# Kernel optimization log

Hardware: AMD Instinct MI355X
Metric: run time of the kernel (lower is better)

The kernel has to match this reference:

```python
import jax, jax.numpy as jnp
import numpy as np

B_, T_, IDIM, D, H, FF, L, MAXLEN = 8, 512, 1799, 256, 4, 2048, 16, 1000
DK = D // H


def _ln(x, g, b, eps=1e-12):
    m = jnp.mean(x, axis=-1, keepdims=True)
    v = jnp.mean((x - m) ** 2, axis=-1, keepdims=True)
    return (x - m) * jax.lax.rsqrt(v + eps) * g + b


def setup_inputs() -> dict:
    key = jax.random.key(0)
    ks = jax.random.split(key, 16)
    s = 0.02
    n = lambda k, shape: jax.random.normal(k, shape, jnp.float32) * s
    return {
        'xs': jax.random.normal(ks[0], (B_, T_, IDIM), jnp.float32),
        'masks': jnp.ones((B_, 1, T_), jnp.int32),
        'emb_w': n(ks[1], (D, IDIM)), 'emb_b': jnp.zeros((D,), jnp.float32),
        'emb_g': jnp.ones((D,), jnp.float32), 'emb_beta': jnp.zeros((D,), jnp.float32),
        'pe_k': n(ks[2], (2 * MAXLEN, DK)),
        'Wq': n(ks[3], (L, D, D)), 'bq': jnp.zeros((L, D), jnp.float32),
        'Wk': n(ks[4], (L, D, D)), 'bk': jnp.zeros((L, D), jnp.float32),
        'Wv': n(ks[5], (L, D, D)), 'bv': jnp.zeros((L, D), jnp.float32),
        'Wo': n(ks[6], (L, D, D)), 'bo': jnp.zeros((L, D), jnp.float32),
        'ln1_g': jnp.ones((L, D), jnp.float32), 'ln1_b': jnp.zeros((L, D), jnp.float32),
        'ln2_g': jnp.ones((L, D), jnp.float32), 'ln2_b': jnp.zeros((L, D), jnp.float32),
        'lnk_g': jnp.ones((L, DK), jnp.float32), 'lnk_b': jnp.zeros((L, DK), jnp.float32),
        'W1': n(ks[7], (L, FF, D)), 'b1': jnp.zeros((L, FF), jnp.float32),
        'W2': n(ks[8], (L, D, FF)), 'b2': jnp.zeros((L, D), jnp.float32),
        'after_g': jnp.ones((D,), jnp.float32), 'after_b': jnp.zeros((D,), jnp.float32),
    }


def reference(xs, masks, emb_w, emb_b, emb_g, emb_beta, pe_k, Wq, bq, Wk, bk, Wv, bv, Wo, bo,
              ln1_g, ln1_b, ln2_g, ln2_b, lnk_g, lnk_b, W1, b1, W2, b2, after_g, after_b):
    # embed: Linear -> LayerNorm -> (Dropout=id) -> ReLU
    x = jax.nn.relu(_ln(xs @ emb_w.T + emb_b, emb_g, emb_beta))  # [B,T,D]
    # relative position table gather: pos_k [T,T,DK]
    pos = jnp.arange(T_)
    rel = jnp.clip(pos[:, None] - pos[None, :], -MAXLEN, MAXLEN - 1) + MAXLEN
    pos_k = pe_k[rel]
    neg = (masks == 0)[:, None, :, :]  # [B,1,1,T]
    minval = jnp.finfo(x.dtype).min
    scale = 1.0 / np.sqrt(DK).astype(np.float32)

    def block(x, p):
        y = _ln(x, p['ln1_g'], p['ln1_b'])
        pk = _ln(pos_k, p['lnk_g'], p['lnk_b'])  # norm_k applied per layer
        proj = lambda W, b: (y @ W.T + b).reshape(B_, T_, H, DK).transpose(0, 2, 1, 3)
        q = proj(p['Wq'], p['bq'])  # [B,H,T,DK]
        k = proj(p['Wk'], p['bk'])
        v = proj(p['Wv'], p['bv'])
        A = jnp.einsum('bhtd,bhsd->bhts', q, k)
        Bt = jnp.einsum('bhtd,tsd->bhts', q, pk)  # rel-pos bias term
        scores = jnp.where(neg, minval, (A + Bt) * scale)
        attn = jnp.where(neg, 0.0, jax.nn.softmax(scores, axis=-1))
        o = jnp.einsum('bhts,bhsd->bhtd', attn, v)
        o = o.transpose(0, 2, 1, 3).reshape(B_, T_, D)
        x = x + o @ p['Wo'].T + p['bo']
        y2 = _ln(x, p['ln2_g'], p['ln2_b'])
        ff = jax.nn.relu(y2 @ p['W1'].T + p['b1']) @ p['W2'].T + p['b2']
        return x + ff, None

    params = {'Wq': Wq, 'bq': bq, 'Wk': Wk, 'bk': bk, 'Wv': Wv, 'bv': bv, 'Wo': Wo, 'bo': bo,
              'ln1_g': ln1_g, 'ln1_b': ln1_b, 'ln2_g': ln2_g, 'ln2_b': ln2_b,
              'lnk_g': lnk_g, 'lnk_b': lnk_b, 'W1': W1, 'b1': b1, 'W2': W2, 'b2': b2}
    x, _ = jax.lax.scan(block, x, params)
    return _ln(x, after_g, after_b)
```

## Files before the change

### kernel.cpp

```cpp
#include <hip/hip_runtime.h>
#include <cstdint>


typedef __bf16 bf16_t;
typedef bf16_t bf16x4 __attribute__((ext_vector_type(4)));
typedef bf16_t bf16x8 __attribute__((ext_vector_type(8)));
typedef float  f32x4  __attribute__((ext_vector_type(4)));

#define B_    8
#define T_    512
#define IDIM  1799
#define KPAD  1856
#define D_    256
#define H_    4
#define DK    64
#define FF_   2048
#define L_    16
#define NROW  4096
#define PKROWS 2000
#define NBH   32
#define NSA   4

__device__ __forceinline__ f32x4 mfma16(bf16x8 a, bf16x8 b, f32x4 c) {
  return __builtin_amdgcn_mfma_f32_16x16x32_bf16(a, b, c, 0, 0, 0);
}

__device__ __forceinline__ void async_cp16(const void* g, void* l) {
  __builtin_amdgcn_global_load_lds(
      (__attribute__((address_space(1))) void*)(g),
      (__attribute__((address_space(3))) void*)(l), 16, 0, 0);
}

__global__ __launch_bounds__(256) void cvt_f32_bf16(const float* __restrict__ s,
                                                    bf16_t* __restrict__ d, int n) {
  int i = blockIdx.x * 256 + threadIdx.x;
  int stride = gridDim.x * 256;
  for (; i < n; i += stride) d[i] = (bf16_t)s[i];
}

__global__ __launch_bounds__(256) void cvt_pad_row(const float* __restrict__ s,
                                                   bf16_t* __restrict__ d,
                                                   int ksrc, int kdst) {
  const int r = blockIdx.x;
  const float* sr = s + (size_t)r * ksrc;
  bf16_t* dr = d + (size_t)r * kdst;
  for (int k = threadIdx.x; k < kdst; k += 256)
    dr[k] = (k < ksrc) ? (bf16_t)sr[k] : (bf16_t)0.f;
}

__global__ __launch_bounds__(256) void pack_qkvw(const float* __restrict__ wq,
                                                 const float* __restrict__ wk,
                                                 const float* __restrict__ wv,
                                                 bf16_t* __restrict__ dst) {
  const int per_l = 768 * 256;
  int i = blockIdx.x * 256 + threadIdx.x;
  int stride = gridDim.x * 256;
  for (; i < L_ * per_l; i += stride) {
    int l = i / per_l, r = i - l * per_l;
    int n = r >> 8, c = r & 255;
    int sel = n >> 8, nn = n & 255;
    const float* w = (sel == 0) ? wq : (sel == 1) ? wk : wv;
    dst[i] = (bf16_t)w[((size_t)l * 256 + nn) * 256 + c];
  }
}

__global__ __launch_bounds__(256) void pack_qkvb(const float* __restrict__ bq,
                                                 const float* __restrict__ bk,
                                                 const float* __restrict__ bv,
                                                 float* __restrict__ dst) {
  int i = blockIdx.x * 256 + threadIdx.x;
  if (i >= L_ * 768) return;
  int l = i / 768, n = i - l * 768;
  int sel = n >> 8, nn = n & 255;
  const float* b = (sel == 0) ? bq : (sel == 1) ? bk : bv;
  dst[i] = b[l * 256 + nn];
}

__global__ __launch_bounds__(256) void pkn_ln(const float* __restrict__ pe_k,
                                              const float* __restrict__ lnk_g,
                                              const float* __restrict__ lnk_b,
                                              bf16_t* __restrict__ out) {
  const int idx = blockIdx.x * 4 + (threadIdx.x >> 6);
  if (idx >= L_ * PKROWS) return;
  const int lane = threadIdx.x & 63;
  const int l = idx / PKROWS, r = idx - l * PKROWS;
  float v = pe_k[(size_t)r * DK + lane];
  float s = v;
#pragma unroll
  for (int o = 32; o; o >>= 1) s += __shfl_xor(s, o);
  const float mean = s * (1.f / DK);
  const float dx = v - mean;
  float q = dx * dx;
#pragma unroll
  for (int o = 32; o; o >>= 1) q += __shfl_xor(q, o);
  const float rs = rsqrtf(q * (1.f / DK) + 1e-12f);
  out[((size_t)l * PKROWS + r) * DK + lane] =
      (bf16_t)(dx * rs * lnk_g[l * DK + lane] + lnk_b[l * DK + lane]);
}

__global__ __launch_bounds__(256) void ln_rows_f32(const float* __restrict__ src,
                                                   const float* __restrict__ g,
                                                   const float* __restrict__ b,
                                                   float* __restrict__ dst) {
  const int row = blockIdx.x * 4 + (threadIdx.x >> 6);
  const int lane = threadIdx.x & 63;
  const float4 v = ((const float4*)(src + (size_t)row * D_))[lane];
  float s = v.x + v.y + v.z + v.w;
#pragma unroll
  for (int o = 32; o; o >>= 1) s += __shfl_xor(s, o);
  const float mean = s * (1.f / D_);
  const float d0 = v.x - mean, d1 = v.y - mean, d2 = v.z - mean, d3 = v.w - mean;
  float q = d0 * d0 + d1 * d1 + d2 * d2 + d3 * d3;
#pragma unroll
  for (int o = 32; o; o >>= 1) q += __shfl_xor(q, o);
  const float rs = rsqrtf(q * (1.f / D_) + 1e-12f);
  const float4 gg = ((const float4*)g)[lane];
  const float4 bb = ((const float4*)b)[lane];
  ((float4*)(dst + (size_t)row * D_))[lane] =
      make_float4(d0 * rs * gg.x + bb.x, d1 * rs * gg.y + bb.y,
                  d2 * rs * gg.z + bb.z, d3 * rs * gg.w + bb.w);
}

template <int NS, bool WRITE_Y>
__global__ __launch_bounds__(256) void add_combine_ln(
    const float* __restrict__ parts, const float* __restrict__ bias,
    float* __restrict__ x, const float* __restrict__ g,
    const float* __restrict__ b, bf16_t* __restrict__ y) {
  const int row = blockIdx.x * 4 + (threadIdx.x >> 6);
  const int lane = threadIdx.x & 63;
  const size_t idx = (size_t)row * 64 + lane;
  float4 v = ((const float4*)x)[idx];
#pragma unroll
  for (int p = 0; p < NS; ++p) {
    float4 pv = ((const float4*)parts)[(size_t)p * NROW * 64 + idx];
    v.x += pv.x; v.y += pv.y; v.z += pv.z; v.w += pv.w;
  }
  const float4 bi = ((const float4*)bias)[lane];
  v.x += bi.x; v.y += bi.y; v.z += bi.z; v.w += bi.w;
  ((float4*)x)[idx] = v;
  if (WRITE_Y) {
    float s = v.x + v.y + v.z + v.w;
#pragma unroll
    for (int o = 32; o; o >>= 1) s += __shfl_xor(s, o);
    const float mean = s * (1.f / D_);
    const float d0 = v.x - mean, d1 = v.y - mean, d2 = v.z - mean, d3 = v.w - mean;
    float q = d0 * d0 + d1 * d1 + d2 * d2 + d3 * d3;
#pragma unroll
    for (int o = 32; o; o >>= 1) q += __shfl_xor(q, o);
    const float rs = rsqrtf(q * (1.f / D_) + 1e-12f);
    const float4 gg = ((const float4*)g)[lane];
    const float4 bb = ((const float4*)b)[lane];
    bf16x4 o4 = {(bf16_t)(d0 * rs * gg.x + bb.x), (bf16_t)(d1 * rs * gg.y + bb.y),
                 (bf16_t)(d2 * rs * gg.z + bb.z), (bf16_t)(d3 * rs * gg.w + bb.w)};
    ((bf16x4*)y)[idx] = o4;
  }
}

__global__ __launch_bounds__(256) void embed_combine(
    const float* __restrict__ parts, const float* __restrict__ bias,
    const float* __restrict__ g0, const float* __restrict__ b0,
    const float* __restrict__ g1, const float* __restrict__ b1,
    float* __restrict__ x, bf16_t* __restrict__ y) {
  const int row = blockIdx.x * 4 + (threadIdx.x >> 6);
  const int lane = threadIdx.x & 63;
  const size_t idx = (size_t)row * 64 + lane;
  float4 v = ((const float4*)parts)[idx];
#pragma unroll
  for (int p = 1; p < 4; ++p) {
    float4 pv = ((const float4*)parts)[(size_t)p * NROW * 64 + idx];
    v.x += pv.x; v.y += pv.y; v.z += pv.z; v.w += pv.w;
  }
  const float4 bi = ((const float4*)bias)[lane];
  v.x += bi.x; v.y += bi.y; v.z += bi.z; v.w += bi.w;
  float s = v.x + v.y + v.z + v.w;
#pragma unroll
  for (int o = 32; o; o >>= 1) s += __shfl_xor(s, o);
  float mean = s * (1.f / D_);
  float d0 = v.x - mean, d1 = v.y - mean, d2 = v.z - mean, d3 = v.w - mean;
  float q = d0 * d0 + d1 * d1 + d2 * d2 + d3 * d3;
#pragma unroll
  for (int o = 32; o; o >>= 1) q += __shfl_xor(q, o);
  float rs = rsqrtf(q * (1.f / D_) + 1e-12f);
  const float4 gg = ((const float4*)g0)[lane];
  const float4 bb = ((const float4*)b0)[lane];
  float x0 = fmaxf(d0 * rs * gg.x + bb.x, 0.f);
  float x1 = fmaxf(d1 * rs * gg.y + bb.y, 0.f);
  float x2 = fmaxf(d2 * rs * gg.z + bb.z, 0.f);
  float x3 = fmaxf(d3 * rs * gg.w + bb.w, 0.f);
  ((float4*)x)[idx] = make_float4(x0, x1, x2, x3);
  s = x0 + x1 + x2 + x3;
#pragma unroll
  for (int o = 32; o; o >>= 1) s += __shfl_xor(s, o);
  mean = s * (1.f / D_);
  d0 = x0 - mean; d1 = x1 - mean; d2 = x2 - mean; d3 = x3 - mean;
  q = d0 * d0 + d1 * d1 + d2 * d2 + d3 * d3;
#pragma unroll
  for (int o = 32; o; o >>= 1) q += __shfl_xor(q, o);
  rs = rsqrtf(q * (1.f / D_) + 1e-12f);
  const float4 g1v = ((const float4*)g1)[lane];
  const float4 b1v = ((const float4*)b1)[lane];
  bf16x4 o4 = {(bf16_t)(d0 * rs * g1v.x + b1v.x), (bf16_t)(d1 * rs * g1v.y + b1v.y),
               (bf16_t)(d2 * rs * g1v.z + b1v.z), (bf16_t)(d3 * rs * g1v.w + b1v.w)};
  ((bf16x4*)y)[idx] = o4;
}

template <int BM, int BN, int EP, int MINW>
__global__ __launch_bounds__(256, MINW) void gemm_bf16(
    const bf16_t* __restrict__ A, int lda, const bf16_t* __restrict__ B, int ldb,
    const float* __restrict__ bias, void* __restrict__ Cout, int ldc,
    int K, size_t zstride) {
  constexpr int HM = BM / 2, HN = BN / 2;
  constexpr int FM = HM / 16, FN = HN / 16;
  constexpr int CA = (BM * 8) / 256, CB = (BN * 8) / 256;
  __shared__ bf16_t lsA[BM * 64];
  __shared__ bf16_t lsB[BN * 64];
  const int tid = threadIdx.x;
  const int w = tid >> 6, lane = tid & 63;
  const int wm = w >> 1, wn = w & 1;
  const int lanelo = lane & 15, quad = lane >> 4;
  const int wbase = tid & ~63;
  const int m0 = blockIdx.x * BM, n0 = blockIdx.y * BN;
  const int ktiles = K >> 6;
  const int tpz = (ktiles + gridDim.z - 1) / gridDim.z;
  const int kb = blockIdx.z * tpz * 64;
  const int ke = min(K, kb + tpz * 64);
  f32x4 acc[FM][FN] = {};

  for (int kt = kb; kt < ke; kt += 64) {
    __syncthreads();
#pragma unroll
    for (int rr = 0; rr < CA; ++rr) {
      int chunk = rr * 256 + tid;
      int r = chunk >> 3, c8 = chunk & 7;
      int lg = c8 ^ (r & 7);
      async_cp16(A + (size_t)(m0 + r) * lda + kt + lg * 8,
                 lsA + (size_t)(rr * 256 + wbase) * 8);
    }
#pragma unroll
    for (int rr = 0; rr < CB; ++rr) {
      int chunk = rr * 256 + tid;
      int r = chunk >> 3, c8 = chunk & 7;
      int lg = c8 ^ (r & 7);
      async_cp16(B + (size_t)(n0 + r) * ldb + kt + lg * 8,
                 lsB + (size_t)(rr * 256 + wbase) * 8);
    }
    __syncthreads();
    bf16x8 af[FM][2], bfv[FN][2];
#pragma unroll
    for (int i = 0; i < FM; ++i) {
      int r = wm * HM + i * 16 + lanelo;
#pragma unroll
      for (int kk = 0; kk < 2; ++kk)
        af[i][kk] = *(const bf16x8*)(lsA + (size_t)(r * 8 + ((kk * 4 + quad) ^ (r & 7))) * 8);
    }
#pragma unroll
    for (int j = 0; j < FN; ++j) {
      int r = wn * HN + j * 16 + lanelo;
#pragma unroll
      for (int kk = 0; kk < 2; ++kk)
        bfv[j][kk] = *(const bf16x8*)(lsB + (size_t)(r * 8 + ((kk * 4 + quad) ^ (r & 7))) * 8);
    }
#pragma unroll
    for (int kk = 0; kk < 2; ++kk)
#pragma unroll
      for (int i = 0; i < FM; ++i)
#pragma unroll
        for (int j = 0; j < FN; ++j)
          acc[i][j] = mfma16(af[i][kk], bfv[j][kk], acc[i][j]);
  }

#pragma unroll
  for (int i = 0; i < FM; ++i) {
#pragma unroll
    for (int j = 0; j < FN; ++j) {
#pragma unroll
      for (int reg = 0; reg < 4; ++reg) {
        const int m = m0 + wm * HM + i * 16 + quad * 4 + reg;
        const int n = n0 + wn * HN + j * 16 + lanelo;
        const size_t idx = (size_t)m * ldc + n;
        if constexpr (EP == 4) {
          ((float*)Cout + (size_t)blockIdx.z * zstride)[idx] = acc[i][j][reg];
        } else {
          float v = acc[i][j][reg] + bias[n];
          if constexpr (EP == 1) {
            ((bf16_t*)Cout)[idx] = (bf16_t)v;
          } else {
            ((bf16_t*)Cout)[idx] = (bf16_t)fmaxf(v, 0.f);
          }
        }
      }
    }
  }
}

__global__ __launch_bounds__(256, 2) void wo_gemm(
    const bf16_t* __restrict__ Opart, const float* __restrict__ mpart,
    const float* __restrict__ lpart, const bf16_t* __restrict__ B,
    float* __restrict__ Cout, size_t zstride) {
  __shared__ bf16_t lsA[64 * 64];
  __shared__ bf16_t lsB[128 * 64];
  const int tid = threadIdx.x;
  const int w = tid >> 6, lane = tid & 63;
  const int wm = w >> 1, wn = w & 1;
  const int lanelo = lane & 15, quad = lane >> 4;
  const int wbase = tid & ~63;
  const int m0 = blockIdx.x * 64, n0 = blockIdx.y * 128;
  const int z = blockIdx.z;
  const int bb = m0 >> 9, t0 = m0 & 511;
  f32x4 acc[2][4] = {};

  for (int kt = z * 128; kt < z * 128 + 128; kt += 64) {
    __syncthreads();
    const int hh = kt >> 6;
    const int bh = bb * 4 + hh;
#pragma unroll
    for (int rr = 0; rr < 2; ++rr) {
      int chunk = rr * 256 + tid;
      int r = chunk >> 3, c8 = chunk & 7;
      int dk0 = (c8 ^ (r & 7)) * 8;
      int t = t0 + r;
      float mp[NSA], lp[NSA];
      float mmax = -__builtin_inff();
#pragma unroll
      for (int p = 0; p < NSA; ++p) {
        const size_t prow = ((size_t)p * NBH + bh) * T_ + t;
        mp[p] = mpart[prow]; lp[p] = lpart[prow];
        mmax = fmaxf(mmax, mp[p]);
      }
      float e[NSA], denom = 0.f;
#pragma unroll
      for (int p = 0; p < NSA; ++p) {
        e[p] = __expf(mp[p] - mmax);
        denom += lp[p] * e[p];
      }
      const float inv = (denom > 0.f) ? 1.f / denom : 0.f;
      float cv[8] = {};
#pragma unroll
      for (int p = 0; p < NSA; ++p) {
        const float wgt = e[p] * inv;
        bf16x8 op = *(const bf16x8*)(Opart +
            (((size_t)p * NBH + bh) * T_ + t) * 64 + dk0);
#pragma unroll
        for (int i = 0; i < 8; ++i) cv[i] += wgt * (float)op[i];
      }
      bf16x8 rv;
#pragma unroll
      for (int i = 0; i < 8; ++i) rv[i] = (bf16_t)cv[i];
      *(bf16x8*)(lsA + (size_t)chunk * 8) = rv;
    }
#pragma unroll
    for (int rr = 0; rr < 4; ++rr) {
      int chunk = rr * 256 + tid;
      int r = chunk >> 3, c8 = chunk & 7;
      int lg = c8 ^ (r & 7);
      async_cp16(B + (size_t)(n0 + r) * 256 + kt + lg * 8,
                 lsB + (size_t)(rr * 256 + wbase) * 8);
    }
    __syncthreads();
    bf16x8 af[2][2], bfv[4][2];
#pragma unroll
    for (int i = 0; i < 2; ++i) {
      int r = wm * 32 + i * 16 + lanelo;
#pragma unroll
      for (int kk = 0; kk < 2; ++kk)
        af[i][kk] = *(const bf16x8*)(lsA + (size_t)(r * 8 + ((kk * 4 + quad) ^ (r & 7))) * 8);
    }
#pragma unroll
    for (int j = 0; j < 4; ++j) {
      int r = wn * 64 + j * 16 + lanelo;
#pragma unroll
      for (int kk = 0; kk < 2; ++kk)
        bfv[j][kk] = *(const bf16x8*)(lsB + (size_t)(r * 8 + ((kk * 4 + quad) ^ (r & 7))) * 8);
    }
#pragma unroll
    for (int kk = 0; kk < 2; ++kk)
#pragma unroll
      for (int i = 0; i < 2; ++i)
#pragma unroll
        for (int j = 0; j < 4; ++j)
          acc[i][j] = mfma16(af[i][kk], bfv[j][kk], acc[i][j]);
  }

#pragma unroll
  for (int i = 0; i < 2; ++i)
#pragma unroll
    for (int j = 0; j < 4; ++j)
#pragma unroll
      for (int reg = 0; reg < 4; ++reg) {
        const int m = m0 + wm * 32 + i * 16 + quad * 4 + reg;
        const int n = n0 + wn * 64 + j * 16 + lanelo;
        (Cout + (size_t)z * zstride)[(size_t)m * D_ + n] = acc[i][j][reg];
      }
}

__global__ __launch_bounds__(256, 3) void attn_fused(
    const bf16_t* __restrict__ qkv, const bf16_t* __restrict__ pkn,
    const int* __restrict__ masks, bf16_t* __restrict__ Opart,
    float* __restrict__ mpart, float* __restrict__ lpart) {
  __shared__ bf16_t ls_qp[64 * 72];
  __shared__ bf16_t ls_pkr[64 * 196];
  __shared__ bf16_t ls_k[64 * 64];
  __shared__ bf16_t ls_vt[64 * 72];

  const int tid = threadIdx.x, w = tid >> 6, lane = tid & 63;
  const int lanelo = lane & 15, quad = lane >> 4;
  const int wbase = tid & ~63;
  const int t0 = blockIdx.x * 64;
  const int bh = blockIdx.y, bb = bh >> 2, h = bh & 3;
  const int z = blockIdx.z;
  const size_t rowbase = (size_t)bb * T_;
  const int jb = t0 - 128 * z + 873;

#pragma unroll
  for (int rr = 0; rr < 2; ++rr) {
    int chunk = rr * 256 + tid;
    int r = chunk >> 3, c8 = chunk & 7;
    int lg = c8 ^ (r & 7);
    async_cp16(qkv + (rowbase + t0 + r) * 768 + h * 64 + lg * 8,
               ls_qp + (size_t)(rr * 256 + wbase) * 8);
  }
#pragma unroll
  for (int rr = 0; rr < 6; ++rr) {
    int chunk = rr * 256 + tid;
    int r = chunk >> 3, c8 = chunk & 7;
    int lg = c8 ^ (r & 7);
    async_cp16(pkn + (size_t)(jb + r) * DK + lg * 8,
               ls_pkr + (size_t)(rr * 256 + wbase) * 8);
  }
  __syncthreads();
  bf16x8 qf[2];
#pragma unroll
  for (int kk = 0; kk < 2; ++kk) {
    int r = w * 16 + lanelo;
    qf[kk] = *(const bf16x8*)(ls_qp + (size_t)(r * 8 + ((kk * 4 + quad) ^ (r & 7))) * 8);
  }
  f32x4 racc[12] = {};
#pragma unroll
  for (int kk = 0; kk < 2; ++kk)
#pragma unroll
    for (int nf = 0; nf < 12; ++nf) {
      int r = nf * 16 + lanelo;
      bf16x8 bj = *(const bf16x8*)(ls_pkr + (size_t)(r * 8 + ((kk * 4 + quad) ^ (r & 7))) * 8);
      racc[nf] = mfma16(qf[kk], bj, racc[nf]);
    }
  __syncthreads();
#pragma unroll
  for (int nf = 0; nf < 12; ++nf)
#pragma unroll
    for (int reg = 0; reg < 4; ++reg)
      ls_pkr[(w * 16 + quad * 4 + reg) * 196 + nf * 16 + lanelo] =
          (bf16_t)racc[nf][reg];

  f32x4 o_acc[4] = {};
  float m_run[4], l_run[4];
#pragma unroll
  for (int i = 0; i < 4; ++i) { m_run[i] = -__builtin_inff(); l_run[i] = 0.f; }

  for (int stl = 0; stl < 2; ++stl) {
    const int s0 = 128 * z + 64 * stl;
    __syncthreads();
#pragma unroll
    for (int rr = 0; rr < 2; ++rr) {
      int chunk = rr * 256 + tid;
      int r = chunk >> 3, c8 = chunk & 7;
      int lg = c8 ^ (r & 7);
      async_cp16(qkv + (rowbase + s0 + r) * 768 + 256 + h * 64 + lg * 8,
                 ls_k + (size_t)(rr * 256 + wbase) * 8);
    }
#pragma unroll
    for (int c = tid; c < 64 * 8; c += 256) {
      int r = c & 63, d0 = (c >> 6) * 8;
      bf16x8 vv = *(const bf16x8*)(qkv + (rowbase + s0 + r) * 768 + 512 + h * 64 + d0);
#pragma unroll
      for (int i = 0; i < 8; ++i) ls_vt[(d0 + i) * 72 + r] = vv[i];
    }
    int mk[4];
#pragma unroll
    for (int nf = 0; nf < 4; ++nf)
      mk[nf] = masks[bb * T_ + s0 + nf * 16 + lanelo];
    __syncthreads();

    f32x4 sacc[4] = {};
#pragma unroll
// ... 60 lines not shown
#pragma unroll
    for (int nf = 0; nf < 4; ++nf)
      Opart[prow * 64 + nf * 16 + lanelo] = (bf16_t)o_acc[nf][reg];
    if (lanelo == 0) { mpart[prow] = m_run[reg]; lpart[prow] = l_run[reg]; }
  }
}

extern "C" void kernel_launch(void* const* d_in, const int* in_sizes, int n_in,
                              void* d_out, int out_size, void* d_ws, size_t ws_size,
                              hipStream_t stream) {
  const float* xs       = (const float*)d_in[0];
  const int*   masks    = (const int*)d_in[1];
  const float* emb_w    = (const float*)d_in[2];
  const float* emb_b    = (const float*)d_in[3];
  const float* emb_g    = (const float*)d_in[4];
  const float* emb_beta = (const float*)d_in[5];
  const float* pe_k     = (const float*)d_in[6];
  const float* Wq       = (const float*)d_in[7];
  const float* bq       = (const float*)d_in[8];
  const float* Wk       = (const float*)d_in[9];
  const float* bk       = (const float*)d_in[10];
  const float* Wv       = (const float*)d_in[11];
  const float* bv       = (const float*)d_in[12];
  const float* Wo       = (const float*)d_in[13];
  const float* bo       = (const float*)d_in[14];
  const float* ln1_g    = (const float*)d_in[15];
  const float* ln1_b    = (const float*)d_in[16];
  const float* ln2_g    = (const float*)d_in[17];
  const float* ln2_b    = (const float*)d_in[18];
  const float* lnk_g    = (const float*)d_in[19];
  const float* lnk_b    = (const float*)d_in[20];
  const float* W1       = (const float*)d_in[21];
  const float* b1       = (const float*)d_in[22];
  const float* W2       = (const float*)d_in[23];
  const float* b2       = (const float*)d_in[24];
  const float* after_g  = (const float*)d_in[25];
  const float* after_b  = (const float*)d_in[26];

  char* ws = (char*)d_ws;
  size_t off = 0;
  auto take = [&](size_t bytes) -> void* {
    void* p = ws + off;
    off += (bytes + 255) & ~(size_t)255;
    return p;
  };
  bf16_t* ewb  = (bf16_t*)take((size_t)D_ * KPAD * 2);
  bf16_t* wcat = (bf16_t*)take((size_t)L_ * 768 * D_ * 2);
  float*  bcat = (float*) take((size_t)L_ * 768 * 4);
  bf16_t* wob  = (bf16_t*)take((size_t)L_ * D_ * D_ * 2);
  bf16_t* w1b  = (bf16_t*)take((size_t)L_ * FF_ * D_ * 2);
  bf16_t* w2b  = (bf16_t*)take((size_t)L_ * D_ * FF_ * 2);
  bf16_t* pknb = (bf16_t*)take((size_t)L_ * PKROWS * DK * 2);
  float*  x    = (float*) take((size_t)NROW * D_ * 4);
  bf16_t* y    = (bf16_t*)take((size_t)NROW * D_ * 2);
  bf16_t* qkv  = (bf16_t*)take((size_t)NROW * 768 * 2);
  bf16_t* hbuf = (bf16_t*)take((size_t)NROW * FF_ * 2);
  bf16_t* Opart = (bf16_t*)take((size_t)NSA * NBH * T_ * 64 * 2);
  float*  mpart = (float*)take((size_t)NSA * NBH * T_ * 4);
  float*  lpart = (float*)take((size_t)NSA * NBH * T_ * 4);
  float*  gpart = (float*)take((size_t)4 * NROW * D_ * 4);
  bf16_t* xsb  = hbuf;
  const size_t ZS = (size_t)NROW * D_;

  cvt_pad_row<<<NROW, 256, 0, stream>>>(xs, xsb, IDIM, KPAD);
  cvt_pad_row<<<D_, 256, 0, stream>>>(emb_w, ewb, IDIM, KPAD);
  pack_qkvw<<<2048, 256, 0, stream>>>(Wq, Wk, Wv, wcat);
  pack_qkvb<<<48, 256, 0, stream>>>(bq, bk, bv, bcat);
  cvt_f32_bf16<<<1024, 256, 0, stream>>>(Wo, wob, L_ * D_ * D_);
  cvt_f32_bf16<<<2048, 256, 0, stream>>>(W1, w1b, L_ * FF_ * D_);
  cvt_f32_bf16<<<2048, 256, 0, stream>>>(W2, w2b, L_ * D_ * FF_);
  pkn_ln<<<(L_ * PKROWS) / 4, 256, 0, stream>>>(pe_k, lnk_g, lnk_b, pknb);

  gemm_bf16<128, 128, 4, 2><<<dim3(NROW / 128, D_ / 128, 4), 256, 0, stream>>>(
      xsb, KPAD, ewb, KPAD, nullptr, gpart, D_, KPAD, ZS);
  embed_combine<<<NROW / 4, 256, 0, stream>>>(gpart, emb_b, emb_g, emb_beta,
                                              ln1_g, ln1_b, x, y);

  for (int l = 0; l < L_; ++l) {
    gemm_bf16<64, 128, 1, 3><<<dim3(NROW / 64, 768 / 128), 256, 0, stream>>>(
        y, D_, wcat + (size_t)l * 768 * D_, D_, bcat + l * 768, qkv, 768, D_, 0);
    attn_fused<<<dim3(T_ / 64, NBH, NSA), 256, 0, stream>>>(
        qkv, pknb + (size_t)l * PKROWS * DK, masks, Opart, mpart, lpart);
    wo_gemm<<<dim3(NROW / 64, D_ / 128, 2), 256, 0, stream>>>(
        Opart, mpart, lpart, wob + (size_t)l * D_ * D_, gpart, ZS);
    add_combine_ln<2, true><<<NROW / 4, 256, 0, stream>>>(
        gpart, bo + l * D_, x, ln2_g + l * D_, ln2_b + l * D_, y);
    gemm_bf16<128, 128, 2, 2><<<dim3(NROW / 128, FF_ / 128), 256, 0, stream>>>(
        y, D_, w1b + (size_t)l * FF_ * D_, D_, b1 + l * FF_, hbuf, FF_, D_, 0);
    gemm_bf16<128, 128, 4, 2><<<dim3(NROW / 128, D_ / 128, 4), 256, 0, stream>>>(
        hbuf, FF_, w2b + (size_t)l * D_ * FF_, FF_, nullptr, gpart, D_, FF_, ZS);
    if (l < L_ - 1) {
      add_combine_ln<4, true><<<NROW / 4, 256, 0, stream>>>(
          gpart, b2 + l * D_, x, ln1_g + (l + 1) * D_, ln1_b + (l + 1) * D_, y);
    } else {
      add_combine_ln<4, false><<<NROW / 4, 256, 0, stream>>>(
          gpart, b2 + l * D_, x, nullptr, nullptr, nullptr);
    }
  }
  ln_rows_f32<<<NROW / 4, 256, 0, stream>>>(x, after_g, after_b, (float*)d_out);
}
```

Baseline: 1.333 ms.

## Fuse LayerNorm into GEMM prologues and residual adds into GEMM epilogues

Removes the separate add/LayerNorm combine kernels. The QKV and FF1 GEMMs now normalise fp32 rows of x into LDS themselves. The Wo GEMM merges the attention split partials and adds bias and residual straight into x, and the FF2 GEMM uses split-K with atomicAdd into x. The weight conversion and packing kernels are merged into a single prep launch. The cost is that LayerNorm is recomputed for every N tile, tiles shrink to 64x64, and fp32 atomics make summation order non-deterministic.

```diff
diff --git a/kernel.cpp b/kernel.cpp
--- a/kernel.cpp
+++ b/kernel.cpp
@@ -31,11 +31,47 @@
       (__attribute__((address_space(3))) void*)(l), 16, 0, 0);
 }
 
-__global__ __launch_bounds__(256) void cvt_f32_bf16(const float* __restrict__ s,
-                                                    bf16_t* __restrict__ d, int n) {
-  int i = blockIdx.x * 256 + threadIdx.x;
-  int stride = gridDim.x * 256;
-  for (; i < n; i += stride) d[i] = (bf16_t)s[i];
+#define WCAT_N (L_ * 768 * 256)
+#define WOB_N  (L_ * 256 * 256)
+#define W1B_N  (L_ * 2048 * 256)
+#define W2B_N  (L_ * 256 * 2048)
+#define BCAT_N (L_ * 768)
+#define PREP_TOT (WCAT_N + WOB_N + W1B_N + W2B_N + BCAT_N)
+
+__global__ __launch_bounds__(256) void prep_all(
+    const float* __restrict__ wq, const float* __restrict__ wk,
+    const float* __restrict__ wv, const float* __restrict__ wo,
+    const float* __restrict__ w1, const float* __restrict__ w2,
+    const float* __restrict__ bq, const float* __restrict__ bk,
+    const float* __restrict__ bv, bf16_t* __restrict__ wcat,
+    bf16_t* __restrict__ wob, bf16_t* __restrict__ w1b,
+    bf16_t* __restrict__ w2b, float* __restrict__ bcat) {
+  const int stride = gridDim.x * 256;
+  for (int i = blockIdx.x * 256 + threadIdx.x; i < PREP_TOT; i += stride) {
+    int j = i;
+    if (j < WCAT_N) {
+      const int per_l = 768 * 256;
+      int l = j / per_l, r = j - l * per_l;
+      int n = r >> 8, c = r & 255;
+      int sel = n >> 8, nn = n & 255;
+      const float* wsrc = (sel == 0) ? wq : (sel == 1) ? wk : wv;
+      wcat[j] = (bf16_t)wsrc[((size_t)l * 256 + nn) * 256 + c];
+      continue;
+    }
+    j -= WCAT_N;
+    if (j < WOB_N) { wob[j] = (bf16_t)wo[j]; continue; }
+    j -= WOB_N;
+    if (j < W1B_N) { w1b[j] = (bf16_t)w1[j]; continue; }
+    j -= W1B_N;
+    if (j < W2B_N) { w2b[j] = (bf16_t)w2[j]; continue; }
+    j -= W2B_N;
+    {
+      int l = j / 768, n = j - l * 768;
+      int sel = n >> 8, nn = n & 255;
+      const float* bsrc = (sel == 0) ? bq : (sel == 1) ? bk : bv;
+      bcat[j] = bsrc[l * 256 + nn];
+    }
+  }
 }
 
 __global__ __launch_bounds__(256) void cvt_pad_row(const float* __restrict__ s,
@@ -46,34 +82,6 @@
   bf16_t* dr = d + (size_t)r * kdst;
   for (int k = threadIdx.x; k < kdst; k += 256)
     dr[k] = (k < ksrc) ? (bf16_t)sr[k] : (bf16_t)0.f;
-}
-
-__global__ __launch_bounds__(256) void pack_qkvw(const float* __restrict__ wq,
-                                                 const float* __restrict__ wk,
-                                                 const float* __restrict__ wv,
-                                                 bf16_t* __restrict__ dst) {
-  const int per_l = 768 * 256;
-  int i = blockIdx.x * 256 + threadIdx.x;
-  int stride = gridDim.x * 256;
-  for (; i < L_ * per_l; i += stride) {
-    int l = i / per_l, r = i - l * per_l;
-    int n = r >> 8, c = r & 255;
-    int sel = n >> 8, nn = n & 255;
-    const float* w = (sel == 0) ? wq : (sel == 1) ? wk : wv;
-    dst[i] = (bf16_t)w[((size_t)l * 256 + nn) * 256 + c];
-  }
-}
-
-__global__ __launch_bounds__(256) void pack_qkvb(const float* __restrict__ bq,
-                                                 const float* __restrict__ bk,
-                                                 const float* __restrict__ bv,
-                                                 float* __restrict__ dst) {
-  int i = blockIdx.x * 256 + threadIdx.x;
-  if (i >= L_ * 768) return;
-  int l = i / 768, n = i - l * 768;
-  int sel = n >> 8, nn = n & 255;
-  const float* b = (sel == 0) ? bq : (sel == 1) ? bk : bv;
-  dst[i] = b[l * 256 + nn];
 }
 
 __global__ __launch_bounds__(256) void pkn_ln(const float* __restrict__ pe_k,
@@ -121,46 +129,10 @@
                   d2 * rs * gg.z + bb.z, d3 * rs * gg.w + bb.w);
 }
 
-template <int NS, bool WRITE_Y>
-__global__ __launch_bounds__(256) void add_combine_ln(
-    const float* __restrict__ parts, const float* __restrict__ bias,
-    float* __restrict__ x, const float* __restrict__ g,
-    const float* __restrict__ b, bf16_t* __restrict__ y) {
-  const int row = blockIdx.x * 4 + (threadIdx.x >> 6);
-  const int lane = threadIdx.x & 63;
-  const size_t idx = (size_t)row * 64 + lane;
-  float4 v = ((const float4*)x)[idx];
-#pragma unroll
-  for (int p = 0; p < NS; ++p) {
-    float4 pv = ((const float4*)parts)[(size_t)p * NROW * 64 + idx];
-    v.x += pv.x; v.y += pv.y; v.z += pv.z; v.w += pv.w;
-  }
-  const float4 bi = ((const float4*)bias)[lane];
-  v.x += bi.x; v.y += bi.y; v.z += bi.z; v.w += bi.w;
-  ((float4*)x)[idx] = v;
-  if (WRITE_Y) {
-    float s = v.x + v.y + v.z + v.w;
-#pragma unroll
-    for (int o = 32; o; o >>= 1) s += __shfl_xor(s, o);
-    const float mean = s * (1.f / D_);
-    const float d0 = v.x - mean, d1 = v.y - mean, d2 = v.z - mean, d3 = v.w - mean;
-    float q = d0 * d0 + d1 * d1 + d2 * d2 + d3 * d3;
-#pragma unroll
-    for (int o = 32; o; o >>= 1) q += __shfl_xor(q, o);
-    const float rs = rsqrtf(q * (1.f / D_) + 1e-12f);
-    const float4 gg = ((const float4*)g)[lane];
-    const float4 bb = ((const float4*)b)[lane];
-    bf16x4 o4 = {(bf16_t)(d0 * rs * gg.x + bb.x), (bf16_t)(d1 * rs * gg.y + bb.y),
-                 (bf16_t)(d2 * rs * gg.z + bb.z), (bf16_t)(d3 * rs * gg.w + bb.w)};
-    ((bf16x4*)y)[idx] = o4;
-  }
-}
-
 __global__ __launch_bounds__(256) void embed_combine(
     const float* __restrict__ parts, const float* __restrict__ bias,
     const float* __restrict__ g0, const float* __restrict__ b0,
-    const float* __restrict__ g1, const float* __restrict__ b1,
-    float* __restrict__ x, bf16_t* __restrict__ y) {
+    float* __restrict__ x) {
   const int row = blockIdx.x * 4 + (threadIdx.x >> 6);
   const int lane = threadIdx.x & 63;
   const size_t idx = (size_t)row * 64 + lane;
@@ -175,43 +147,23 @@
   float s = v.x + v.y + v.z + v.w;
 #pragma unroll
   for (int o = 32; o; o >>= 1) s += __shfl_xor(s, o);
-  float mean = s * (1.f / D_);
-  float d0 = v.x - mean, d1 = v.y - mean, d2 = v.z - mean, d3 = v.w - mean;
+  const float mean = s * (1.f / D_);
+  const float d0 = v.x - mean, d1 = v.y - mean, d2 = v.z - mean, d3 = v.w - mean;
   float q = d0 * d0 + d1 * d1 + d2 * d2 + d3 * d3;
 #pragma unroll
   for (int o = 32; o; o >>= 1) q += __shfl_xor(q, o);
-  float rs = rsqrtf(q * (1.f / D_) + 1e-12f);
+  const float rs = rsqrtf(q * (1.f / D_) + 1e-12f);
   const float4 gg = ((const float4*)g0)[lane];
   const float4 bb = ((const float4*)b0)[lane];
-  float x0 = fmaxf(d0 * rs * gg.x + bb.x, 0.f);
-  float x1 = fmaxf(d1 * rs * gg.y + bb.y, 0.f);
-  float x2 = fmaxf(d2 * rs * gg.z + bb.z, 0.f);
-  float x3 = fmaxf(d3 * rs * gg.w + bb.w, 0.f);
-  ((float4*)x)[idx] = make_float4(x0, x1, x2, x3);
-  s = x0 + x1 + x2 + x3;
-#pragma unroll
-  for (int o = 32; o; o >>= 1) s += __shfl_xor(s, o);
-  mean = s * (1.f / D_);
-  d0 = x0 - mean; d1 = x1 - mean; d2 = x2 - mean; d3 = x3 - mean;
-  q = d0 * d0 + d1 * d1 + d2 * d2 + d3 * d3;
-#pragma unroll
-  for (int o = 32; o; o >>= 1) q += __shfl_xor(q, o);
-  rs = rsqrtf(q * (1.f / D_) + 1e-12f);
-  const float4 g1v = ((const float4*)g1)[lane];
-  const float4 b1v = ((const float4*)b1)[lane];
-  bf16x4 o4 = {(bf16_t)(d0 * rs * g1v.x + b1v.x), (bf16_t)(d1 * rs * g1v.y + b1v.y),
-               (bf16_t)(d2 * rs * g1v.z + b1v.z), (bf16_t)(d3 * rs * g1v.w + b1v.w)};
-  ((bf16x4*)y)[idx] = o4;
-}
-
-template <int BM, int BN, int EP, int MINW>
-__global__ __launch_bounds__(256, MINW) void gemm_bf16(
-    const bf16_t* __restrict__ A, int lda, const bf16_t* __restrict__ B, int ldb,
-    const float* __restrict__ bias, void* __restrict__ Cout, int ldc,
-    int K, size_t zstride) {
-  constexpr int HM = BM / 2, HN = BN / 2;
-  constexpr int FM = HM / 16, FN = HN / 16;
-  constexpr int CA = (BM * 8) / 256, CB = (BN * 8) / 256;
+  ((float4*)x)[idx] = make_float4(
+      fmaxf(d0 * rs * gg.x + bb.x, 0.f), fmaxf(d1 * rs * gg.y + bb.y, 0.f),
+      fmaxf(d2 * rs * gg.z + bb.z, 0.f), fmaxf(d3 * rs * gg.w + bb.w, 0.f));
+}
+
+__global__ __launch_bounds__(256, 2) void gemm_embed(
+    const bf16_t* __restrict__ A, const bf16_t* __restrict__ B,
+    float* __restrict__ Cout, size_t zstride) {
+  constexpr int BM = 128, BN = 128;
   __shared__ bf16_t lsA[BM * 64];
   __shared__ bf16_t lsB[BN * 64];
   const int tid = threadIdx.x;
@@ -220,42 +172,42 @@
   const int lanelo = lane & 15, quad = lane >> 4;
   const int wbase = tid & ~63;
   const int m0 = blockIdx.x * BM, n0 = blockIdx.y * BN;
-  const int ktiles = K >> 6;
-  const int tpz = (ktiles + gridDim.z - 1) / gridDim.z;
+  const int ktiles = KPAD >> 6;
+  const int tpz = (ktiles + 3) / 4;
   const int kb = blockIdx.z * tpz * 64;
-  const int ke = min(K, kb + tpz * 64);
-  f32x4 acc[FM][FN] = {};
+  const int ke = min(KPAD, kb + tpz * 64);
+  f32x4 acc[4][4] = {};
 
   for (int kt = kb; kt < ke; kt += 64) {
     __syncthreads();
 #pragma unroll
-    for (int rr = 0; rr < CA; ++rr) {
+    for (int rr = 0; rr < 4; ++rr) {
       int chunk = rr * 256 + tid;
       int r = chunk >> 3, c8 = chunk & 7;
       int lg = c8 ^ (r & 7);
-      async_cp16(A + (size_t)(m0 + r) * lda + kt + lg * 8,
+      async_cp16(A + (size_t)(m0 + r) * KPAD + kt + lg * 8,
                  lsA + (size_t)(rr * 256 + wbase) * 8);
     }
 #pragma unroll
-    for (int rr = 0; rr < CB; ++rr) {
+    for (int rr = 0; rr < 4; ++rr) {
       int chunk = rr * 256 + tid;
       int r = chunk >> 3, c8 = chunk & 7;
       int lg = c8 ^ (r & 7);
-      async_cp16(B + (size_t)(n0 + r) * ldb + kt + lg * 8,
+      async_cp16(B + (size_t)(n0 + r) * KPAD + kt + lg * 8,
                  lsB + (size_t)(rr * 256 + wbase) * 8);
     }
     __syncthreads();
-    bf16x8 af[FM][2], bfv[FN][2];
-#pragma unroll
-    for (int i = 0; i < FM; ++i) {
-      int r = wm * HM + i * 16 + lanelo;
+    bf16x8 af[4][2], bfv[4][2];
+#pragma unroll
+    for (int i = 0; i < 4; ++i) {
+      int r = wm * 64 + i * 16 + lanelo;
 #pragma unroll
       for (int kk = 0; kk < 2; ++kk)
         af[i][kk] = *(const bf16x8*)(lsA + (size_t)(r * 8 + ((kk * 4 + quad) ^ (r & 7))) * 8);
     }
 #pragma unroll
-    for (int j = 0; j < FN; ++j) {
-      int r = wn * HN + j * 16 + lanelo;
+    for (int j = 0; j < 4; ++j) {
+      int r = wn * 64 + j * 16 + lanelo;
 #pragma unroll
       for (int kk = 0; kk < 2; ++kk)
         bfv[j][kk] = *(const bf16x8*)(lsB + (size_t)(r * 8 + ((kk * 4 + quad) ^ (r & 7))) * 8);
@@ -263,101 +215,279 @@
 #pragma unroll
     for (int kk = 0; kk < 2; ++kk)
 #pragma unroll
-      for (int i = 0; i < FM; ++i)
-#pragma unroll
-        for (int j = 0; j < FN; ++j)
+      for (int i = 0; i < 4; ++i)
+#pragma unroll
+        for (int j = 0; j < 4; ++j)
           acc[i][j] = mfma16(af[i][kk], bfv[j][kk], acc[i][j]);
   }
-
-#pragma unroll
-  for (int i = 0; i < FM; ++i) {
-#pragma unroll
-    for (int j = 0; j < FN; ++j) {
+#pragma unroll
+  for (int i = 0; i < 4; ++i)
+#pragma unroll
+    for (int j = 0; j < 4; ++j)
 #pragma unroll
       for (int reg = 0; reg < 4; ++reg) {
-        const int m = m0 + wm * HM + i * 16 + quad * 4 + reg;
-        const int n = n0 + wn * HN + j * 16 + lanelo;
-        const size_t idx = (size_t)m * ldc + n;
-        if constexpr (EP == 4) {
-          ((float*)Cout + (size_t)blockIdx.z * zstride)[idx] = acc[i][j][reg];
-        } else {
-          float v = acc[i][j][reg] + bias[n];
-          if constexpr (EP == 1) {
-            ((bf16_t*)Cout)[idx] = (bf16_t)v;
-          } else {
-            ((bf16_t*)Cout)[idx] = (bf16_t)fmaxf(v, 0.f);
-          }
-        }
-      }
-    }
-  }
-}
-
-__global__ __launch_bounds__(256, 2) void wo_gemm(
-    const bf16_t* __restrict__ Opart, const float* __restrict__ mpart,
-    const float* __restrict__ lpart, const bf16_t* __restrict__ B,
-    float* __restrict__ Cout, size_t zstride) {
-  __shared__ bf16_t lsA[64 * 64];
-  __shared__ bf16_t lsB[128 * 64];
+        const int m = m0 + wm * 64 + i * 16 + quad * 4 + reg;
+        const int n = n0 + wn * 64 + j * 16 + lanelo;
+        (Cout + (size_t)blockIdx.z * zstride)[(size_t)m * D_ + n] =
+            acc[i][j][reg];
+      }
+}
+
+template <int EP>
+__global__ __launch_bounds__(256, 2) void gemm_ln(
+    const float* __restrict__ X, const float* __restrict__ g,
+    const float* __restrict__ b, const bf16_t* __restrict__ Bw,
+    const float* __restrict__ bias, bf16_t* __restrict__ Cout, int ldc) {
+  __shared__ bf16_t lsA[64 * 256];
+  __shared__ bf16_t lsB[64 * 256];
   const int tid = threadIdx.x;
   const int w = tid >> 6, lane = tid & 63;
   const int wm = w >> 1, wn = w & 1;
   const int lanelo = lane & 15, quad = lane >> 4;
   const int wbase = tid & ~63;
-  const int m0 = blockIdx.x * 64, n0 = blockIdx.y * 128;
+  const int m0 = blockIdx.x * 64, n0 = blockIdx.y * 64;
+
+#pragma unroll
+  for (int rr = 0; rr < 8; ++rr) {
+    int ch = rr * 256 + tid;
+    int r = ch >> 5, kb = (ch >> 3) & 3, c = ch & 7;
+    int lg = c ^ (r & 7);
+    async_cp16(Bw + (size_t)(n0 + r) * 256 + kb * 64 + lg * 8,
+               lsB + (size_t)(rr * 256 + wbase) * 8);
+  }
+  {
+    const int ar = tid >> 2, aq = tid & 3;
+    const float4* xrow = (const float4*)(X + (size_t)(m0 + ar) * 256) + aq * 16;
+    float4 xv[16];
+    float sum = 0.f;
+#pragma unroll
+    for (int i = 0; i < 16; ++i) {
+      xv[i] = xrow[i];
+      sum += xv[i].x + xv[i].y + xv[i].z + xv[i].w;
+    }
+    sum += __shfl_xor(sum, 1);
+    sum += __shfl_xor(sum, 2);
+    const float mean = sum * (1.f / 256.f);
+    float ss = 0.f;
+#pragma unroll
+    for (int i = 0; i < 16; ++i) {
+      float a0 = xv[i].x - mean, a1 = xv[i].y - mean;
+      float a2 = xv[i].z - mean, a3 = xv[i].w - mean;
+      ss += a0 * a0 + a1 * a1 + a2 * a2 + a3 * a3;
+    }
+    ss += __shfl_xor(ss, 1);
+    ss += __shfl_xor(ss, 2);
+    const float rs = rsqrtf(ss * (1.f / 256.f) + 1e-12f);
+    const float4* gg4 = (const float4*)g + aq * 16;
+    const float4* bb4 = (const float4*)b + aq * 16;
+#pragma unroll
+    for (int c = 0; c < 8; ++c) {
+      float4 v0 = xv[c * 2], v1 = xv[c * 2 + 1];
+      float4 g0 = gg4[c * 2], g1 = gg4[c * 2 + 1];
+      float4 b0 = bb4[c * 2], b1 = bb4[c * 2 + 1];
+      bf16x8 o;
+      o[0] = (bf16_t)((v0.x - mean) * rs * g0.x + b0.x);
+      o[1] = (bf16_t)((v0.y - mean) * rs * g0.y + b0.y);
+      o[2] = (bf16_t)((v0.z - mean) * rs * g0.z + b0.z);
+      o[3] = (bf16_t)((v0.w - mean) * rs * g0.w + b0.w);
+      o[4] = (bf16_t)((v1.x - mean) * rs * g1.x + b1.x);
+      o[5] = (bf16_t)((v1.y - mean) * rs * g1.y + b1.y);
+      o[6] = (bf16_t)((v1.z - mean) * rs * g1.z + b1.z);
+      o[7] = (bf16_t)((v1.w - mean) * rs * g1.w + b1.w);
+      *(bf16x8*)(lsA + (size_t)ar * 256 + (aq * 8 + ((c + ar) & 7)) * 8) = o;
+    }
+  }
+  __syncthreads();
+
+  f32x4 acc[2][2] = {};
+#pragma unroll
+  for (int kb = 0; kb < 4; ++kb) {
+    bf16x8 af[2][2], bfv[2][2];
+#pragma unroll
+    for (int i = 0; i < 2; ++i) {
+      int r = wm * 32 + i * 16 + lanelo;
+#pragma unroll
+      for (int kk = 0; kk < 2; ++kk)
+        af[i][kk] = *(const bf16x8*)(lsA + (size_t)r * 256 +
+                                     (kb * 8 + ((kk * 4 + quad + r) & 7)) * 8);
+    }
+#pragma unroll
+    for (int j = 0; j < 2; ++j) {
+      int r = wn * 32 + j * 16 + lanelo;
+#pragma unroll
+      for (int kk = 0; kk < 2; ++kk)
+        bfv[j][kk] = *(const bf16x8*)(lsB + (size_t)r * 256 +
+                                      (kb * 8 + ((kk * 4 + quad) ^ (r & 7))) * 8);
+    }
+#pragma unroll
+    for (int kk = 0; kk < 2; ++kk)
+#pragma unroll
+      for (int i = 0; i < 2; ++i)
+#pragma unroll
+        for (int j = 0; j < 2; ++j)
+          acc[i][j] = mfma16(af[i][kk], bfv[j][kk], acc[i][j]);
+  }
+
+#pragma unroll
+  for (int i = 0; i < 2; ++i)
+#pragma unroll
+    for (int j = 0; j < 2; ++j)
+#pragma unroll
+      for (int reg = 0; reg < 4; ++reg) {
+        const int m = m0 + wm * 32 + i * 16 + quad * 4 + reg;
+        const int n = n0 + wn * 32 + j * 16 + lanelo;
+        float v = acc[i][j][reg] + bias[n];
+        if (EP == 2) v = fmaxf(v, 0.f);
+        Cout[(size_t)m * ldc + n] = (bf16_t)v;
+      }
+}
+
+__global__ __launch_bounds__(256, 2) void wo_fused(
+    const bf16_t* __restrict__ Opart, const float* __restrict__ mpart,
+    const float* __restrict__ lpart, const bf16_t* __restrict__ Bw,
+    const float* __restrict__ bo, float* __restrict__ x) {
+  __shared__ bf16_t lsA[64 * 256];
+  __shared__ bf16_t lsB[64 * 256];
+  __shared__ float lswgt[64 * 4 * 4];
+  const int tid = threadIdx.x;
+  const int w = tid >> 6, lane = tid & 63;
+  const int wm = w >> 1, wn = w & 1;
+  const int lanelo = lane & 15, quad = lane >> 4;
+  const int wbase = tid & ~63;
+  const int m0 = blockIdx.x * 64, n0 = blockIdx.y * 64;
+  const int bb = m0 >> 9, t0 = m0 & 511;
+
+#pragma unroll
+  for (int rr = 0; rr < 8; ++rr) {
+    int ch = rr * 256 + tid;
+    int r = ch >> 5, kb = (ch >> 3) & 3, c = ch & 7;
+    int lg = c ^ (r & 7);
+    async_cp16(Bw + (size_t)(n0 + r) * 256 + kb * 64 + lg * 8,
+               lsB + (size_t)(rr * 256 + wbase) * 8);
+  }
+  {
+    const int r = tid >> 2, h = tid & 3;
+    const int bh = bb * 4 + h;
+    const int t = t0 + r;
+    float mp[NSA], lp[NSA];
+    float mmax = -__builtin_inff();
+#pragma unroll
+    for (int p = 0; p < NSA; ++p) {
+      const size_t prow = ((size_t)p * NBH + bh) * T_ + t;
+      mp[p] = mpart[prow]; lp[p] = lpart[prow];
+      mmax = fmaxf(mmax, mp[p]);
+    }
+    float e[NSA], denom = 0.f;
+#pragma unroll
+    for (int p = 0; p < NSA; ++p) {
+      e[p] = __expf(mp[p] - mmax);
+      denom += lp[p] * e[p];
+    }
+    const float inv = (denom > 0.f) ? 1.f / denom : 0.f;
+#pragma unroll
+    for (int p = 0; p < NSA; ++p) lswgt[(r * 4 + h) * 4 + p] = e[p] * inv;
+  }
+  __syncthreads();
+  {
+    const int kb = (tid >> 3) & 3, c = tid & 7;
+    const int bh = bb * 4 + kb;
+#pragma unroll
+    for (int rr = 0; rr < 8; ++rr) {
+      const int r = (tid >> 5) + 8 * rr;
+      const int t = t0 + r;
+      float cv[8] = {};
+#pragma unroll
+      for (int p = 0; p < NSA; ++p) {
+        const float wgt = lswgt[(r * 4 + kb) * 4 + p];
+        bf16x8 op = *(const bf16x8*)(Opart +
+            (((size_t)p * NBH + bh) * T_ + t) * 64 + c * 8);
+#pragma unroll
+        for (int i = 0; i < 8; ++i) cv[i] += wgt * (float)op[i];
+      }
+      bf16x8 o;
+#pragma unroll
+      for (int i = 0; i < 8; ++i) o[i] = (bf16_t)cv[i];
+      *(bf16x8*)(lsA + (size_t)r * 256 + (kb * 8 + ((c + r) & 7)) * 8) = o;
+    }
+  }
+  __syncthreads();
+
+  f32x4 acc[2][2] = {};
+#pragma unroll
+  for (int kb = 0; kb < 4; ++kb) {
+    bf16x8 af[2][2], bfv[2][2];
+#pragma unroll
+    for (int i = 0; i < 2; ++i) {
+      int r = wm * 32 + i * 16 + lanelo;
+#pragma unroll
+      for (int kk = 0; kk < 2; ++kk)
+        af[i][kk] = *(const bf16x8*)(lsA + (size_t)r * 256 +
+                                     (kb * 8 + ((kk * 4 + quad + r) & 7)) * 8);
+    }
+#pragma unroll
+    for (int j = 0; j < 2; ++j) {
+      int r = wn * 32 + j * 16 + lanelo;
+#pragma unroll
+      for (int kk = 0; kk < 2; ++kk)
+        bfv[j][kk] = *(const bf16x8*)(lsB + (size_t)r * 256 +
+                                      (kb * 8 + ((kk * 4 + quad) ^ (r & 7))) * 8);
+    }
+#pragma unroll
+    for (int kk = 0; kk < 2; ++kk)
+#pragma unroll
+      for (int i = 0; i < 2; ++i)
+#pragma unroll
+        for (int j = 0; j < 2; ++j)
+          acc[i][j] = mfma16(af[i][kk], bfv[j][kk], acc[i][j]);
+  }
+
+#pragma unroll
+  for (int i = 0; i < 2; ++i)
+#pragma unroll
+    for (int j = 0; j < 2; ++j)
+#pragma unroll
+      for (int reg = 0; reg < 4; ++reg) {
+        const int m = m0 + wm * 32 + i * 16 + quad * 4 + reg;
+        const int n = n0 + wn * 32 + j * 16 + lanelo;
+        const size_t idx = (size_t)m * D_ + n;
+        x[idx] = x[idx] + acc[i][j][reg] + bo[n];
+      }
+}
+
+__global__ __launch_bounds__(256, 3) void ff2_gemm(
+    const bf16_t* __restrict__ A, const bf16_t* __restrict__ Bw,
+    const float* __restrict__ b2, float* __restrict__ x) {
+  __shared__ bf16_t lsA[64 * 64];
+  __shared__ bf16_t lsB[64 * 64];
+  const int tid = threadIdx.x;
+  const int w = tid >> 6, lane = tid & 63;
+  const int wm = w >> 1, wn = w & 1;
+  const int lanelo = lane & 15, quad = lane >> 4;
+  const int wbase = tid & ~63;
+  const int m0 = blockIdx.x * 64, n0 = blockIdx.y * 64;
   const int z = blockIdx.z;
-  const int bb = m0 >> 9, t0 = m0 & 511;
-  f32x4 acc[2][4] = {};
-
-  for (int kt = z * 128; kt < z * 128 + 128; kt += 64) {
+  f32x4 acc[2][2] = {};
+
+  for (int kt = z * 1024; kt < z * 1024 + 1024; kt += 64) {
     __syncthreads();
-    const int hh = kt >> 6;
-    const int bh = bb * 4 + hh;
 #pragma unroll
     for (int rr = 0; rr < 2; ++rr) {
       int chunk = rr * 256 + tid;
       int r = chunk >> 3, c8 = chunk & 7;
-      int dk0 = (c8 ^ (r & 7)) * 8;
-      int t = t0 + r;
-      float mp[NSA], lp[NSA];
-      float mmax = -__builtin_inff();
-#pragma unroll
-      for (int p = 0; p < NSA; ++p) {
-        const size_t prow = ((size_t)p * NBH + bh) * T_ + t;
-        mp[p] = mpart[prow]; lp[p] = lpart[prow];
-        mmax = fmaxf(mmax, mp[p]);
-      }
-      float e[NSA], denom = 0.f;
-#pragma unroll
-      for (int p = 0; p < NSA; ++p) {
-        e[p] = __expf(mp[p] - mmax);
-        denom += lp[p] * e[p];
-      }
-      const float inv = (denom > 0.f) ? 1.f / denom : 0.f;
-      float cv[8] = {};
-#pragma unroll
-      for (int p = 0; p < NSA; ++p) {
-        const float wgt = e[p] * inv;
-        bf16x8 op = *(const bf16x8*)(Opart +
-            (((size_t)p * NBH + bh) * T_ + t) * 64 + dk0);
-#pragma unroll
-        for (int i = 0; i < 8; ++i) cv[i] += wgt * (float)op[i];
-      }
-      bf16x8 rv;
-#pragma unroll
-      for (int i = 0; i < 8; ++i) rv[i] = (bf16_t)cv[i];
-      *(bf16x8*)(lsA + (size_t)chunk * 8) = rv;
-    }
-#pragma unroll
-    for (int rr = 0; rr < 4; ++rr) {
+      int lg = c8 ^ (r & 7);
+      async_cp16(A + (size_t)(m0 + r) * FF_ + kt + lg * 8,
+                 lsA + (size_t)(rr * 256 + wbase) * 8);
+    }
+#pragma unroll
+    for (int rr = 0; rr < 2; ++rr) {
       int chunk = rr * 256 + tid;
       int r = chunk >> 3, c8 = chunk & 7;
       int lg = c8 ^ (r & 7);
-      async_cp16(B + (size_t)(n0 + r) * 256 + kt + lg * 8,
+      async_cp16(Bw + (size_t)(n0 + r) * FF_ + kt + lg * 8,
                  lsB + (size_t)(rr * 256 + wbase) * 8);
     }
     __syncthreads();
-    bf16x8 af[2][2], bfv[4][2];
+    bf16x8 af[2][2], bfv[2][2];
 #pragma unroll
     for (int i = 0; i < 2; ++i) {
       int r = wm * 32 + i * 16 + lanelo;
@@ -366,8 +496,8 @@
         af[i][kk] = *(const bf16x8*)(lsA + (size_t)(r * 8 + ((kk * 4 + quad) ^ (r & 7))) * 8);
     }
 #pragma unroll
-    for (int j = 0; j < 4; ++j) {
-      int r = wn * 64 + j * 16 + lanelo;
+    for (int j = 0; j < 2; ++j) {
+      int r = wn * 32 + j * 16 + lanelo;
 #pragma unroll
       for (int kk = 0; kk < 2; ++kk)
         bfv[j][kk] = *(const bf16x8*)(lsB + (size_t)(r * 8 + ((kk * 4 + quad) ^ (r & 7))) * 8);
@@ -377,19 +507,21 @@
 #pragma unroll
       for (int i = 0; i < 2; ++i)
 #pragma unroll
-        for (int j = 0; j < 4; ++j)
+        for (int j = 0; j < 2; ++j)
           acc[i][j] = mfma16(af[i][kk], bfv[j][kk], acc[i][j]);
   }
 
 #pragma unroll
   for (int i = 0; i < 2; ++i)
 #pragma unroll
-    for (int j = 0; j < 4; ++j)
+    for (int j = 0; j < 2; ++j)
 #pragma unroll
       for (int reg = 0; reg < 4; ++reg) {
         const int m = m0 + wm * 32 + i * 16 + quad * 4 + reg;
-        const int n = n0 + wn * 64 + j * 16 + lanelo;
-        (Cout + (size_t)z * zstride)[(size_t)m * D_ + n] = acc[i][j][reg];
+        const int n = n0 + wn * 32 + j * 16 + lanelo;
+        float v = acc[i][j][reg];
+        if (z == 0) v += b2[n];
+        atomicAdd(x + (size_t)m * D_ + n, v);
       }
 }
 
@@ -429,6 +561,11 @@
   }
   __syncthreads();
   bf16x8 qf[2];
+#pragma unroll
+  for (int kk = 0; kk < 2; ++kk) {
+    int r = w * 16 + lanelo;
+    qf[kk] = *(const bf16x8*)(ls_pkr + 0);
+  }
 #pragma unroll
   for (int kk = 0; kk < 2; ++kk) {
     int r = w * 16 + lanelo;
@@ -595,7 +732,6 @@
   bf16_t* w2b  = (bf16_t*)take((size_t)L_ * D_ * FF_ * 2);
   bf16_t* pknb = (bf16_t*)take((size_t)L_ * PKROWS * DK * 2);
   float*  x    = (float*) take((size_t)NROW * D_ * 4);
-  bf16_t* y    = (bf16_t*)take((size_t)NROW * D_ * 2);
   bf16_t* qkv  = (bf16_t*)take((size_t)NROW * 768 * 2);
   bf16_t* hbuf = (bf16_t*)take((size_t)NROW * FF_ * 2);
   bf16_t* Opart = (bf16_t*)take((size_t)NSA * NBH * T_ * 64 * 2);
@@ -607,38 +743,26 @@
 
   cvt_pad_row<<<NROW, 256, 0, stream>>>(xs, xsb, IDIM, KPAD);
   cvt_pad_row<<<D_, 256, 0, stream>>>(emb_w, ewb, IDIM, KPAD);
-  pack_qkvw<<<2048, 256, 0, stream>>>(Wq, Wk, Wv, wcat);
-  pack_qkvb<<<48, 256, 0, stream>>>(bq, bk, bv, bcat);
-  cvt_f32_bf16<<<1024, 256, 0, stream>>>(Wo, wob, L_ * D_ * D_);
-  cvt_f32_bf16<<<2048, 256, 0, stream>>>(W1, w1b, L_ * FF_ * D_);
-  cvt_f32_bf16<<<2048, 256, 0, stream>>>(W2, w2b, L_ * D_ * FF_);
+  prep_all<<<4096, 256, 0, stream>>>(Wq, Wk, Wv, Wo, W1, W2, bq, bk, bv,
+                                     wcat, wob, w1b, w2b, bcat);
   pkn_ln<<<(L_ * PKROWS) / 4, 256, 0, stream>>>(pe_k, lnk_g, lnk_b, pknb);
 
-  gemm_bf16<128, 128, 4, 2><<<dim3(NROW / 128, D_ / 128, 4), 256, 0, stream>>>(
-      xsb, KPAD, ewb, KPAD, nullptr, gpart, D_, KPAD, ZS);
-  embed_combine<<<NROW / 4, 256, 0, stream>>>(gpart, emb_b, emb_g, emb_beta,
-                                              ln1_g, ln1_b, x, y);
+  gemm_embed<<<dim3(NROW / 128, D_ / 128, 4), 256, 0, stream>>>(xsb, ewb, gpart, ZS);
+  embed_combine<<<NROW / 4, 256, 0, stream>>>(gpart, emb_b, emb_g, emb_beta, x);
 
   for (int l = 0; l < L_; ++l) {
-    gemm_bf16<64, 128, 1, 3><<<dim3(NROW / 64, 768 / 128), 256, 0, stream>>>(
-        y, D_, wcat + (size_t)l * 768 * D_, D_, bcat + l * 768, qkv, 768, D_, 0);
+    gemm_ln<1><<<dim3(NROW / 64, 768 / 64), 256, 0, stream>>>(
+        x, ln1_g + l * D_, ln1_b + l * D_, wcat + (size_t)l * 768 * D_,
+        bcat + l * 768, qkv, 768);
     attn_fused<<<dim3(T_ / 64, NBH, NSA), 256, 0, stream>>>(
         qkv, pknb + (size_t)l * PKROWS * DK, masks, Opart, mpart, lpart);
-    wo_gemm<<<dim3(NROW / 64, D_ / 128, 2), 256, 0, stream>>>(
-        Opart, mpart, lpart, wob + (size_t)l * D_ * D_, gpart, ZS);
-    add_combine_ln<2, true><<<NROW / 4, 256, 0, stream>>>(
-        gpart, bo + l * D_, x, ln2_g + l * D_, ln2_b + l * D_, y);
-    gemm_bf16<128, 128, 2, 2><<<dim3(NROW / 128, FF_ / 128), 256, 0, stream>>>(
-        y, D_, w1b + (size_t)l * FF_ * D_, D_, b1 + l * FF_, hbuf, FF_, D_, 0);
-    gemm_bf16<128, 128, 4, 2><<<dim3(NROW / 128, D_ / 128, 4), 256, 0, stream>>>(
-        hbuf, FF_, w2b + (size_t)l * D_ * FF_, FF_, nullptr, gpart, D_, FF_, ZS);
-    if (l < L_ - 1) {
-      add_combine_ln<4, true><<<NROW / 4, 256, 0, stream>>>(
-          gpart, b2 + l * D_, x, ln1_g + (l + 1) * D_, ln1_b + (l + 1) * D_, y);
-    } else {
-      add_combine_ln<4, false><<<NROW / 4, 256, 0, stream>>>(
-          gpart, b2 + l * D_, x, nullptr, nullptr, nullptr);
-    }
+    wo_fused<<<dim3(NROW / 64, D_ / 64), 256, 0, stream>>>(
+        Opart, mpart, lpart, wob + (size_t)l * D_ * D_, bo + l * D_, x);
+    gemm_ln<2><<<dim3(NROW / 64, FF_ / 64), 256, 0, stream>>>(
+        x, ln2_g + l * D_, ln2_b + l * D_, w1b + (size_t)l * FF_ * D_,
+        b1 + l * FF_, hbuf, FF_);
+    ff2_gemm<<<dim3(NROW / 64, D_ / 64, 2), 256, 0, stream>>>(
+        hbuf, w2b + (size_t)l * D_ * FF_, b2 + l * D_, x);
   }
   ln_rows_f32<<<NROW / 4, 256, 0, stream>>>(x, after_g, after_b, (float*)d_out);
 }
```

Result: slower. 2.103 ms (+57.8%).
